# Kernel optimization log

Hardware: AMD Instinct MI355X
Metric: run time of the kernel (lower is better)

Reference implementation:

```python
import jax, jax.numpy as jnp
import numpy as np

PAD = 0
V, D = 50000, 300
MUS = np.array([-0.9, -0.7, -0.5, -0.3, -0.1, 0.1, 0.3, 0.5, 0.7, 0.9, 1.0], dtype=np.float32)
SIGMAS = np.array([0.1] * 10 + [0.001], dtype=np.float32)


def setup_inputs() -> dict:
    key = jax.random.key(0)
    k1, k2, k3, k4, k5, k6, k7 = jax.random.split(key, 7)
    B, Q, T = 256, 16, 1024
    return {
        "posdoc": jax.random.randint(k1, (B, T), 0, V),
        "negdoc": jax.random.randint(k2, (B, T), 0, V),
        "query": jax.random.randint(k3, (B, Q), 0, V),
        "query_idf": jax.random.normal(k4, (B, Q), dtype=jnp.float32),
        "emb": jax.random.normal(k5, (V, D), dtype=jnp.float32) * 0.1,
        "mus": jnp.asarray(MUS),
        "sigmas": jnp.asarray(SIGMAS),
        "W": jax.random.normal(k6, (11, 1), dtype=jnp.float32) * 0.3,
        "b": jax.random.normal(k7, (1,), dtype=jnp.float32) * 0.01,
    }


def _get_score(doc_tok, query_tok, emb, mus, sigmas, W, b):
    q = emb[query_tok]                                    # [B,Q,D]
    d = emb[doc_tok]                                      # [B,T,D]
    qn = q / (jnp.linalg.norm(q, axis=-1, keepdims=True) + 1e-9)
    dn = d / (jnp.linalg.norm(d, axis=-1, keepdims=True) + 1e-9)
    sim = jnp.einsum('bqd,btd->bqt', qn, dn)              # cosine simmat [B,Q,T]
    pair_mask = (query_tok != PAD)[:, :, None] & (doc_tok != PAD)[:, None, :]
    sim = sim * pair_mask                                 # zero out pad pairs
    # RBF kernel bank: [B,K,Q,T]
    diff = sim[:, None, :, :] - mus[None, :, None, None]
    k = jnp.exp(-0.5 * diff * diff / (sigmas[None, :, None, None] ** 2))
    doc_k = jnp.sum(k, axis=3)                            # [B,K,Q]
    qmask = jnp.sum(sim, axis=2) != 0.0                   # [B,Q]
    log_k = jnp.where(qmask[:, None, :], jnp.log(doc_k + 1e-6), 0.0)
    query_k = jnp.sum(log_k, axis=2)                      # [B,K]
    return (query_k @ W + b)[:, 0]                        # [B]


def reference(posdoc, negdoc, query, query_idf, emb, mus, sigmas, W, b):
    pos = _get_score(posdoc, query, emb, mus, sigmas, W, b)
    neg = _get_score(negdoc, query, emb, mus, sigmas, W, b)
    return jnp.stack([pos, neg], axis=1)                  # [B,2]
```

## Files before the change

kernel.cpp:

```cpp
#include <hip/hip_runtime.h>
#include <math.h>

#define BQ 16
#define TT 1024
#define DD 300
#define KK 11
#define ND4 75
#define KPAD 320
#define NCH 4

typedef unsigned short u16;
typedef unsigned char u8;
typedef long long i64;
typedef float f32x4 __attribute__((ext_vector_type(4)));

__device__ __forceinline__ unsigned f2e4m3(float f) {
    unsigned u = __float_as_uint(f);
    unsigned s = (u >> 24) & 0x80u;
    float a = fabsf(f);
    unsigned code;
    if (a < 0.015625f) {
        code = (unsigned)(int)rintf(a * 512.0f);
    } else {
        unsigned au = u & 0x7fffffffu;
        au += 0x7ffffu + ((au >> 20) & 1u);
        int e32 = (int)(au >> 23) - 127;
        code = ((unsigned)(e32 + 7) << 3) | ((au >> 20) & 7u);
    }
    return s | code;
}

__global__ __launch_bounds__(256) void knrm_norm_table(
    const float* __restrict__ emb, u8* __restrict__ table, int V)
{
    const int tid = threadIdx.x;
    const int sub = tid & 15;
    const int row = blockIdx.x * 16 + (tid >> 4);
    if (row >= V) return;

    const float4* __restrict__ src = (const float4*)(emb + (size_t)row * DD);
    float4 v[5];
    float ssq = 0.f;
    #pragma unroll
    for (int it = 0; it < 5; ++it) {
        int j = sub + 16 * it;
        if (j < ND4) {
            v[it] = src[j];
            ssq += v[it].x * v[it].x + v[it].y * v[it].y
                 + v[it].z * v[it].z + v[it].w * v[it].w;
        } else {
            v[it] = make_float4(0.f, 0.f, 0.f, 0.f);
        }
    }
    #pragma unroll
    for (int off = 8; off; off >>= 1) ssq += __shfl_xor(ssq, off, 16);
    const float inv = (row == 0) ? 0.f : 1.f / (sqrtf(ssq) + 1e-9f);

    unsigned* __restrict__ dst = (unsigned*)(table + (size_t)row * KPAD);
    #pragma unroll
    for (int it = 0; it < 5; ++it) {
        int j = sub + 16 * it;
        unsigned w = f2e4m3(v[it].x * inv)
                   | (f2e4m3(v[it].y * inv) << 8)
                   | (f2e4m3(v[it].z * inv) << 16)
                   | (f2e4m3(v[it].w * inv) << 24);
        dst[j] = w;
    }
}

__global__ __launch_bounds__(256, 4) void knrm_mfma(
    const int* __restrict__ posdoc, const int* __restrict__ negdoc,
    const int* __restrict__ query,
    const u8* __restrict__ table,
    const float* __restrict__ mus, const float* __restrict__ sigmas,
    float* __restrict__ part)
{
    __shared__ float red[4][BQ][12];

    const int bid   = blockIdx.x;
    const int pair  = bid >> 2;
    const int chunk = bid & 3;
    const int bb    = pair >> 1;
    const int* __restrict__ doc = (pair & 1) ? negdoc : posdoc;
    const int tid  = threadIdx.x;
    const int lane = tid & 63;
    const int wave = tid >> 6;
    const int quad = lane >> 4;
    const int m    = lane & 15;

    const int qtok = query[bb * BQ + m];
    const i64* __restrict__ ap = (const i64*)(table + (size_t)qtok * KPAD + quad * 8);
    i64 afr[10];
    #pragma unroll
    for (int ks = 0; ks < 10; ++ks) afr[ks] = ap[ks * 4];

    const int tbase = bb * TT + chunk * 256 + wave * 64 + m;
    int toks[4];
    #pragma unroll
    for (int t = 0; t < 4; ++t) toks[t] = doc[tbase + t * 16];

    float muk[10], ck[10];
    #pragma unroll
    for (int k = 0; k < 10; ++k) {
        muk[k] = mus[k];
        float sg = sigmas[k];
        ck[k] = -0.72134752f / (sg * sg);
    }

    float vacc[12][4];
    #pragma unroll
    for (int v = 0; v < 12; ++v)
        #pragma unroll
        for (int r = 0; r < 4; ++r) vacc[v][r] = 0.f;

    #pragma unroll
    for (int tp = 0; tp < 2; ++tp) {
        const i64* __restrict__ bp0 =
            (const i64*)(table + (size_t)toks[2 * tp]     * KPAD + quad * 8);
        const i64* __restrict__ bp1 =
            (const i64*)(table + (size_t)toks[2 * tp + 1] * KPAD + quad * 8);
        i64 b0[10], b1[10];
        #pragma unroll
        for (int ks = 0; ks < 10; ++ks) { b0[ks] = bp0[ks * 4]; b1[ks] = bp1[ks * 4]; }

        f32x4 acc0 = {0.f, 0.f, 0.f, 0.f};
        f32x4 acc1 = {0.f, 0.f, 0.f, 0.f};
        #pragma unroll
        for (int ks = 0; ks < 10; ++ks) {
            acc0 = __builtin_amdgcn_mfma_f32_16x16x32_fp8_fp8(afr[ks], b0[ks], acc0, 0, 0, 0);
            acc1 = __builtin_amdgcn_mfma_f32_16x16x32_fp8_fp8(afr[ks], b1[ks], acc1, 0, 0, 0);
        }

        #pragma unroll
        for (int r = 0; r < 4; ++r) {
            float s0 = acc0[r], s1 = acc1[r];
            vacc[11][r] += s0 + s1;
            vacc[10][r] += (s0 > 0.9f ? 1.f : 0.f)
                         + (s1 > 0.9f ? 1.f : 0.f);
            #pragma unroll
            for (int k = 0; k < 10; ++k) {
                float d0 = s0 - muk[k], d1 = s1 - muk[k];
                vacc[k][r] += __builtin_amdgcn_exp2f(ck[k] * d0 * d0)
                            + __builtin_amdgcn_exp2f(ck[k] * d1 * d1);
            }
        }
    }

    #pragma unroll
    for (int r = 0; r < 4; ++r) {
        #pragma unroll
        for (int off = 8; off; off >>= 1)
            #pragma unroll
            for (int v = 0; v < 12; ++v)
                vacc[v][r] += __shfl_down(vacc[v][r], off, 16);
        if (m == 0) {
            int q = quad * 4 + r;
            #pragma unroll
            for (int v = 0; v < 12; ++v) red[wave][q][v] = vacc[v][r];
        }
    }
    __syncthreads();

    if (tid < 192) {
        int v = tid >> 4, q = tid & 15;
        float sum = red[0][q][v] + red[1][q][v] + red[2][q][v] + red[3][q][v];
        part[((size_t)bid * 12 + v) * BQ + q] = sum;
    }
}

__global__ __launch_bounds__(256) void knrm_partial(
    const int* __restrict__ posdoc, const int* __restrict__ negdoc,
    const int* __restrict__ query,
    const float* __restrict__ emb,
    const float* __restrict__ mus, const float* __restrict__ sigmas,
    float* __restrict__ ws)
{
    __shared__ __align__(16) float qs[BQ * DD];
    __shared__ float qscale[BQ];

    const int bid   = blockIdx.x;
    const int pair  = bid >> 2;
    const int chunk = bid & 3;
    const int bb    = pair >> 1;
    const int sel   = pair & 1;
    const int* __restrict__ doc = sel ? negdoc : posdoc;
    const int tid  = threadIdx.x;
    const int lane = tid & 63;
    const int wave = tid >> 6;

    float4* qs4 = (float4*)qs;
    for (int idx = tid; idx < BQ * ND4; idx += 256) {
        int q   = idx / ND4;
        int c   = idx - q * ND4;
        int tok = query[bb * BQ + q];
        qs4[idx] = ((const float4*)(emb + (size_t)tok * DD))[c];
    }
    __syncthreads();
    {
        int q = tid >> 4, sub = tid & 15;
        float ssq = 0.f;
        for (int i = sub; i < DD; i += 16) { float v = qs[q * DD + i]; ssq += v * v; }
        #pragma unroll
        for (int off = 8; off; off >>= 1) ssq += __shfl_down(ssq, off, 16);
        if (sub == 0) {
            int tok = query[bb * BQ + q];
            qscale[q] = (tok == 0) ? 0.f : 1.f / (sqrtf(ssq) + 1e-9f);
        }
    }
    __syncthreads();
    for (int idx = tid; idx < BQ * ND4; idx += 256) {
        int q = idx / ND4;
        float sc = qscale[q];
        float4 v = qs4[idx];
        v.x *= sc; v.y *= sc; v.z *= sc; v.w *= sc;
        qs4[idx] = v;
    }
    __syncthreads();

    const int tok = doc[bb * TT + chunk * 256 + tid];
    const float4* __restrict__ rowp = (const float4*)(emb + (size_t)tok * DD);
    float acc[BQ];
    #pragma unroll
    for (int q = 0; q < BQ; ++q) acc[q] = 0.f;
    float dss = 0.f;
    #pragma unroll 5
    for (int d4 = 0; d4 < ND4; ++d4) {
        float4 dv = rowp[d4];
        dss += dv.x * dv.x + dv.y * dv.y + dv.z * dv.z + dv.w * dv.w;
        #pragma unroll
        for (int q = 0; q < BQ; ++q) {
            float4 qv = qs4[q * ND4 + d4];
            acc[q] += dv.x * qv.x + dv.y * qv.y + dv.z * qv.z + dv.w * qv.w;
        }
    }
    const float invd = (tok == 0) ? 0.f : 1.f / (sqrtf(dss) + 1e-9f);

    float muk[KK], ck[KK];
    #pragma unroll
    for (int k = 0; k < KK; ++k) {
        muk[k] = mus[k];
        float sg = sigmas[k];
        ck[k] = -0.72134752f / (sg * sg);
    }
    __syncthreads();
    float* red = qs;
    const int grp = wave * 4 + (lane >> 4);
    const bool wr = (lane & 15) == 0;
    for (int q = 0; q < BQ; ++q) {
        float s = acc[q] * invd;
        float vals[12];
        vals[11] = s;
        #pragma unroll
        for (int k = 0; k < KK; ++k) {
            float d = s - muk[k];
            vals[k] = __builtin_amdgcn_exp2f(ck[k] * d * d);
        }
        #pragma unroll
        for (int off = 8; off; off >>= 1)
            #pragma unroll
            for (int v = 0; v < 12; ++v)
                vals[v] += __shfl_down(vals[v], off, 16);
        if (wr) {
            #pragma unroll
            for (int v = 0; v < 12; ++v) red[(grp * BQ + q) * 12 + v] = vals[v];
        }
    }
    __syncthreads();
    if (tid < 192) {
        int v = tid >> 4, q = tid & 15;
        float sum = 0.f;
        #pragma unroll
        for (int g = 0; g < 16; ++g) sum += red[(g * BQ + q) * 12 + v];
        ws[((size_t)(pair * 4 + chunk) * 12 + v) * BQ + q] = sum;
    }
}

__global__ __launch_bounds__(192) void knrm_final(
    const float* __restrict__ part,
    const float* __restrict__ Wv, const float* __restrict__ bv,
    float* __restrict__ out, int nchunk)
{
    __shared__ float dock[12 * BQ];
    __shared__ float lsum[KK];
    const int pair = blockIdx.x;
    const int tid  = threadIdx.x;
    {
        int v = tid >> 4, q = tid & 15;
        float sum = 0.f;
        for (int c = 0; c < nchunk; ++c)
            sum += part[((size_t)(pair * nchunk + c) * 12 + v) * BQ + q];
        dock[v * BQ + q] = sum;
    }
    __syncthreads();
    if (tid < 176) {
        int k = tid >> 4, q = tid & 15;
        float qm = dock[11 * BQ + q];
        float lv = (qm != 0.0f) ? logf(dock[k * BQ + q] + 1e-6f) : 0.f;
        #pragma unroll
        for (int off = 8; off; off >>= 1) lv += __shfl_down(lv, off, 16);
        if (q == 0) lsum[k] = lv;
    }
    __syncthreads();
    if (tid == 0) {
        float sc = bv[0];
        #pragma unroll
        for (int k = 0; k < KK; ++k) sc += lsum[k] * Wv[k];
        out[pair] = sc;
    }
}

extern "C" void kernel_launch(void* const* d_in, const int* in_sizes, int n_in,
                              void* d_out, int out_size, void* d_ws, size_t ws_size,
                              hipStream_t stream) {
    const int*   posdoc = (const int*)  d_in[0];
    const int*   negdoc = (const int*)  d_in[1];
    const int*   query  = (const int*)  d_in[2];
    const float* emb    = (const float*)d_in[4];
    const float* mus    = (const float*)d_in[5];
    const float* sigmas = (const float*)d_in[6];
    const float* Wv     = (const float*)d_in[7];
    const float* bv     = (const float*)d_in[8];
    float* out = (float*)d_out;

    const int V = in_sizes[4] / DD;
    const size_t table_bytes = (size_t)V * KPAD;
    const size_t part_bytes  = (size_t)512 * NCH * 12 * BQ * sizeof(float);

    if (ws_size >= table_bytes + part_bytes) {
        u8*    table = (u8*)d_ws;
        float* part  = (float*)((char*)d_ws + table_bytes);
        knrm_norm_table<<<dim3((V + 15) / 16), dim3(256), 0, stream>>>(emb, table, V);
        knrm_mfma<<<dim3(512 * NCH), dim3(256), 0, stream>>>(
            posdoc, negdoc, query, table, mus, sigmas, part);
        knrm_final<<<dim3(512), dim3(192), 0, stream>>>(part, Wv, bv, out, NCH);
    } else {
        float* part = (float*)d_ws;
        knrm_partial<<<dim3(512 * 4), dim3(256), 0, stream>>>(
            posdoc, negdoc, query, emb, mus, sigmas, part);
        knrm_final<<<dim3(512), dim3(192), 0, stream>>>(part, Wv, bv, out, 4);
    }
}
```

Before: 155.3 us.

## Permute FP8 table layout for 16-byte loads and double-buffer doc fragments

The normalized FP8 embedding table is written in a permuted order so each lane's MFMA K-fragments sit contiguously. Each lane can then fetch them with five 16-byte loads instead of ten 8-byte strided loads. The doc-token loop now handles one token group at a time and software-prefetches the next group's fragments into a second register buffer while the current MFMAs and exp work run. This trades the two independent MFMA chains of the old loop for one chain per token, which could expose more MFMA latency, but it aims to cut load instruction count and improve load/compute overlap.

Measured after the change: 181.1 us. 16.6% more time.

```diff
diff --git a/kernel.cpp b/kernel.cpp
--- a/kernel.cpp
+++ b/kernel.cpp
@@ -13,6 +13,7 @@
 typedef unsigned char u8;
 typedef long long i64;
 typedef float f32x4 __attribute__((ext_vector_type(4)));
+typedef long long i64x2 __attribute__((ext_vector_type(2)));
 
 __device__ __forceinline__ unsigned f2e4m3(float f) {
     unsigned u = __float_as_uint(f);
@@ -64,7 +65,10 @@
                    | (f2e4m3(v[it].y * inv) << 8)
                    | (f2e4m3(v[it].z * inv) << 16)
                    | (f2e4m3(v[it].w * inv) << 24);
-        dst[j] = w;
+        int quad = (j >> 1) & 3;
+        int ks   = j >> 3;
+        int d    = quad * 20 + ks * 2 + (j & 1);
+        dst[d] = w;
     }
 }
 
@@ -88,16 +92,20 @@
     const int quad = lane >> 4;
     const int m    = lane & 15;
 
-    const int qtok = query[bb * BQ + m];
-    const i64* __restrict__ ap = (const i64*)(table + (size_t)qtok * KPAD + quad * 8);
-    i64 afr[10];
-    #pragma unroll
-    for (int ks = 0; ks < 10; ++ks) afr[ks] = ap[ks * 4];
-
     const int tbase = bb * TT + chunk * 256 + wave * 64 + m;
     int toks[4];
     #pragma unroll
     for (int t = 0; t < 4; ++t) toks[t] = doc[tbase + t * 16];
+    const i64x2* __restrict__ bp[4];
+    #pragma unroll
+    for (int t = 0; t < 4; ++t)
+        bp[t] = (const i64x2*)(table + (size_t)toks[t] * KPAD + quad * 80);
+
+    const int qtok = query[bb * BQ + m];
+    const i64x2* __restrict__ ap = (const i64x2*)(table + (size_t)qtok * KPAD + quad * 80);
+    i64x2 afr[5];
+    #pragma unroll
+    for (int g = 0; g < 5; ++g) afr[g] = ap[g];
 
     float muk[10], ck[10];
     #pragma unroll
@@ -113,35 +121,32 @@
         #pragma unroll
         for (int r = 0; r < 4; ++r) vacc[v][r] = 0.f;
 
-    #pragma unroll
-    for (int tp = 0; tp < 2; ++tp) {
-        const i64* __restrict__ bp0 =
-            (const i64*)(table + (size_t)toks[2 * tp]     * KPAD + quad * 8);
-        const i64* __restrict__ bp1 =
-            (const i64*)(table + (size_t)toks[2 * tp + 1] * KPAD + quad * 8);
-        i64 b0[10], b1[10];
-        #pragma unroll
-        for (int ks = 0; ks < 10; ++ks) { b0[ks] = bp0[ks * 4]; b1[ks] = bp1[ks * 4]; }
-
-        f32x4 acc0 = {0.f, 0.f, 0.f, 0.f};
-        f32x4 acc1 = {0.f, 0.f, 0.f, 0.f};
-        #pragma unroll
-        for (int ks = 0; ks < 10; ++ks) {
-            acc0 = __builtin_amdgcn_mfma_f32_16x16x32_fp8_fp8(afr[ks], b0[ks], acc0, 0, 0, 0);
-            acc1 = __builtin_amdgcn_mfma_f32_16x16x32_fp8_fp8(afr[ks], b1[ks], acc1, 0, 0, 0);
-        }
-
+    i64x2 bbuf[2][5];
+    #pragma unroll
+    for (int g = 0; g < 5; ++g) bbuf[0][g] = bp[0][g];
+
+    #pragma unroll
+    for (int t = 0; t < 4; ++t) {
+        const int cur = t & 1;
+        if (t < 3) {
+            #pragma unroll
+            for (int g = 0; g < 5; ++g) bbuf[cur ^ 1][g] = bp[t + 1][g];
+        }
+        f32x4 acc = {0.f, 0.f, 0.f, 0.f};
+        #pragma unroll
+        for (int g = 0; g < 5; ++g) {
+            acc = __builtin_amdgcn_mfma_f32_16x16x32_fp8_fp8(afr[g].x, bbuf[cur][g].x, acc, 0, 0, 0);
+            acc = __builtin_amdgcn_mfma_f32_16x16x32_fp8_fp8(afr[g].y, bbuf[cur][g].y, acc, 0, 0, 0);
+        }
         #pragma unroll
         for (int r = 0; r < 4; ++r) {
-            float s0 = acc0[r], s1 = acc1[r];
-            vacc[11][r] += s0 + s1;
-            vacc[10][r] += (s0 > 0.9f ? 1.f : 0.f)
-                         + (s1 > 0.9f ? 1.f : 0.f);
+            float s = acc[r];
+            vacc[11][r] += s;
+            vacc[10][r] += (s > 0.9f ? 1.f : 0.f);
             #pragma unroll
             for (int k = 0; k < 10; ++k) {
-                float d0 = s0 - muk[k], d1 = s1 - muk[k];
-                vacc[k][r] += __builtin_amdgcn_exp2f(ck[k] * d0 * d0)
-                            + __builtin_amdgcn_exp2f(ck[k] * d1 * d1);
+                float d = s - muk[k];
+                vacc[k][r] += __builtin_amdgcn_exp2f(ck[k] * d * d);
             }
         }
     }
```

## Software-pipeline doc tile loads with inline asm and one-wave-per-row norm table

Applied to the files above, without the earlier changes.

The MFMA kernel now issues doc-embedding loads with explicit inline-asm global loads into two rotating register buffers and uses manual vmcnt waits, so the next tile's loads are in flight while the current tile's MFMAs and RBF exponentials run. Occupancy hint drops from 4 to 3 blocks per SIMD to make room for the extra buffered registers. The norm-table kernel is reorganised to one wave per embedding row with a full-wave shuffle reduction, and now explicitly zeroes the padding bytes. The risks are fewer resident waves, and fragile manual vmcnt accounting that depends on the compiler not inserting other loads in between.

Result: faster. 151.1 us (-2.7%).

```diff
diff --git a/kernel.cpp b/kernel.cpp
--- a/kernel.cpp
+++ b/kernel.cpp
@@ -30,45 +30,54 @@
     return s | code;
 }
 
+template<int OFF>
+__device__ __forceinline__ void gload8(i64& dst, const u8* p) {
+    asm volatile("global_load_dwordx2 %0, %1, off offset:%2"
+                 : "=v"(dst) : "v"(p), "i"(OFF));
+}
+
+#define ISSUE_TILE(B, P)                                                    \
+    gload8<0>((B)[0], P);   gload8<32>((B)[1], P);  gload8<64>((B)[2], P);  \
+    gload8<96>((B)[3], P);  gload8<128>((B)[4], P); gload8<160>((B)[5], P); \
+    gload8<192>((B)[6], P); gload8<224>((B)[7], P); gload8<256>((B)[8], P); \
+    gload8<288>((B)[9], P);
+
+#define TILE_WAIT(NSTR, B)                                                  \
+    asm volatile("s_waitcnt vmcnt(" NSTR ")"                                \
+        : "+v"((B)[0]), "+v"((B)[1]), "+v"((B)[2]), "+v"((B)[3]),           \
+          "+v"((B)[4]), "+v"((B)[5]), "+v"((B)[6]), "+v"((B)[7]),           \
+          "+v"((B)[8]), "+v"((B)[9]))
+
 __global__ __launch_bounds__(256) void knrm_norm_table(
     const float* __restrict__ emb, u8* __restrict__ table, int V)
 {
-    const int tid = threadIdx.x;
-    const int sub = tid & 15;
-    const int row = blockIdx.x * 16 + (tid >> 4);
-    if (row >= V) return;
-
-    const float4* __restrict__ src = (const float4*)(emb + (size_t)row * DD);
-    float4 v[5];
-    float ssq = 0.f;
-    #pragma unroll
-    for (int it = 0; it < 5; ++it) {
-        int j = sub + 16 * it;
-        if (j < ND4) {
-            v[it] = src[j];
-            ssq += v[it].x * v[it].x + v[it].y * v[it].y
-                 + v[it].z * v[it].z + v[it].w * v[it].w;
-        } else {
-            v[it] = make_float4(0.f, 0.f, 0.f, 0.f);
-        }
-    }
-    #pragma unroll
-    for (int off = 8; off; off >>= 1) ssq += __shfl_xor(ssq, off, 16);
-    const float inv = (row == 0) ? 0.f : 1.f / (sqrtf(ssq) + 1e-9f);
-
-    unsigned* __restrict__ dst = (unsigned*)(table + (size_t)row * KPAD);
-    #pragma unroll
-    for (int it = 0; it < 5; ++it) {
-        int j = sub + 16 * it;
-        unsigned w = f2e4m3(v[it].x * inv)
-                   | (f2e4m3(v[it].y * inv) << 8)
-                   | (f2e4m3(v[it].z * inv) << 16)
-                   | (f2e4m3(v[it].w * inv) << 24);
-        dst[j] = w;
-    }
-}
-
-__global__ __launch_bounds__(256, 4) void knrm_mfma(
+    const int w    = (blockIdx.x * 256 + threadIdx.x) >> 6;
+    const int lane = threadIdx.x & 63;
+    if (w >= V) return;
+
+    const float4* __restrict__ src = (const float4*)(emb + (size_t)w * DD);
+    float4 v = make_float4(0.f, 0.f, 0.f, 0.f);
+    float4 v2 = v;
+    if (lane < ND4) v = src[lane];
+    if (lane < ND4 - 64) v2 = src[64 + lane];
+    float ssq = v.x * v.x + v.y * v.y + v.z * v.z + v.w * v.w
+              + v2.x * v2.x + v2.y * v2.y + v2.z * v2.z + v2.w * v2.w;
+    #pragma unroll
+    for (int off = 32; off; off >>= 1) ssq += __shfl_xor(ssq, off);
+    const float inv = (w == 0) ? 0.f : 1.f / (sqrtf(ssq) + 1e-9f);
+
+    unsigned* __restrict__ dst = (unsigned*)(table + (size_t)w * KPAD);
+    unsigned p = f2e4m3(v.x * inv) | (f2e4m3(v.y * inv) << 8)
+               | (f2e4m3(v.z * inv) << 16) | (f2e4m3(v.w * inv) << 24);
+    dst[lane] = (lane < ND4) ? p : 0u;
+    if (lane < 16) {
+        unsigned p2 = f2e4m3(v2.x * inv) | (f2e4m3(v2.y * inv) << 8)
+                    | (f2e4m3(v2.z * inv) << 16) | (f2e4m3(v2.w * inv) << 24);
+        dst[64 + lane] = (lane < ND4 - 64) ? p2 : 0u;
+    }
+}
+
+__global__ __launch_bounds__(256, 3) void knrm_mfma(
     const int* __restrict__ posdoc, const int* __restrict__ negdoc,
     const int* __restrict__ query,
     const u8* __restrict__ table,
@@ -88,16 +97,20 @@
     const int quad = lane >> 4;
     const int m    = lane & 15;
 
+    const int tbase = bb * TT + chunk * 256 + wave * 64 + m;
+    int toks[4];
+    #pragma unroll
+    for (int t = 0; t < 4; ++t) toks[t] = doc[tbase + t * 16];
+    const u8* bp0 = table + (size_t)toks[0] * KPAD + quad * 8;
+    const u8* bp1 = table + (size_t)toks[1] * KPAD + quad * 8;
+    const u8* bp2 = table + (size_t)toks[2] * KPAD + quad * 8;
+    const u8* bp3 = table + (size_t)toks[3] * KPAD + quad * 8;
+
     const int qtok = query[bb * BQ + m];
     const i64* __restrict__ ap = (const i64*)(table + (size_t)qtok * KPAD + quad * 8);
     i64 afr[10];
     #pragma unroll
     for (int ks = 0; ks < 10; ++ks) afr[ks] = ap[ks * 4];
-
-    const int tbase = bb * TT + chunk * 256 + wave * 64 + m;
-    int toks[4];
-    #pragma unroll
-    for (int t = 0; t < 4; ++t) toks[t] = doc[tbase + t * 16];
 
     float muk[10], ck[10];
     #pragma unroll
@@ -113,38 +126,44 @@
         #pragma unroll
         for (int r = 0; r < 4; ++r) vacc[v][r] = 0.f;
 
-    #pragma unroll
-    for (int tp = 0; tp < 2; ++tp) {
-        const i64* __restrict__ bp0 =
-            (const i64*)(table + (size_t)toks[2 * tp]     * KPAD + quad * 8);
-        const i64* __restrict__ bp1 =
-            (const i64*)(table + (size_t)toks[2 * tp + 1] * KPAD + quad * 8);
-        i64 b0[10], b1[10];
-        #pragma unroll
-        for (int ks = 0; ks < 10; ++ks) { b0[ks] = bp0[ks * 4]; b1[ks] = bp1[ks * 4]; }
-
-        f32x4 acc0 = {0.f, 0.f, 0.f, 0.f};
-        f32x4 acc1 = {0.f, 0.f, 0.f, 0.f};
-        #pragma unroll
-        for (int ks = 0; ks < 10; ++ks) {
-            acc0 = __builtin_amdgcn_mfma_f32_16x16x32_fp8_fp8(afr[ks], b0[ks], acc0, 0, 0, 0);
-            acc1 = __builtin_amdgcn_mfma_f32_16x16x32_fp8_fp8(afr[ks], b1[ks], acc1, 0, 0, 0);
-        }
-
-        #pragma unroll
-        for (int r = 0; r < 4; ++r) {
-            float s0 = acc0[r], s1 = acc1[r];
-            vacc[11][r] += s0 + s1;
-            vacc[10][r] += (s0 > 0.9f ? 1.f : 0.f)
-                         + (s1 > 0.9f ? 1.f : 0.f);
-            #pragma unroll
-            for (int k = 0; k < 10; ++k) {
-                float d0 = s0 - muk[k], d1 = s1 - muk[k];
-                vacc[k][r] += __builtin_amdgcn_exp2f(ck[k] * d0 * d0)
-                            + __builtin_amdgcn_exp2f(ck[k] * d1 * d1);
-            }
-        }
-    }
+    asm volatile("s_waitcnt vmcnt(0)"
+        : "+v"(afr[0]), "+v"(afr[1]), "+v"(afr[2]), "+v"(afr[3]), "+v"(afr[4]),
+          "+v"(afr[5]), "+v"(afr[6]), "+v"(afr[7]), "+v"(afr[8]), "+v"(afr[9]));
+
+    i64 ba[10], bbuf[10];
+    ISSUE_TILE(ba, bp0);
+    ISSUE_TILE(bbuf, bp1);
+
+    #define COMPUTE_TILE(B)                                                        \
+    {                                                                              \
+        f32x4 acc = {0.f, 0.f, 0.f, 0.f};                                          \
+        _Pragma("unroll")                                                          \
+        for (int g = 0; g < 10; ++g)                                               \
+            acc = __builtin_amdgcn_mfma_f32_16x16x32_fp8_fp8(afr[g], (B)[g], acc, 0, 0, 0); \
+        _Pragma("unroll")                                                          \
+        for (int r = 0; r < 4; ++r) {                                              \
+            float s = acc[r];                                                      \
+            vacc[11][r] += s;                                                      \
+            vacc[10][r] += (s > 0.9f ? 1.f : 0.f);                                 \
+            _Pragma("unroll")                                                      \
+            for (int k = 0; k < 10; ++k) {                                         \
+                float d = s - muk[k];                                              \
+                vacc[k][r] += __builtin_amdgcn_exp2f(ck[k] * d * d);               \
+            }                                                                      \
+        }                                                                          \
+    }
+
+    TILE_WAIT("10", ba);
+    COMPUTE_TILE(ba);
+    ISSUE_TILE(ba, bp2);
+    TILE_WAIT("10", bbuf);
+    COMPUTE_TILE(bbuf);
+    ISSUE_TILE(bbuf, bp3);
+    TILE_WAIT("10", ba);
+    COMPUTE_TILE(ba);
+    TILE_WAIT("0", bbuf);
+    COMPUTE_TILE(bbuf);
+    #undef COMPUTE_TILE
 
     #pragma unroll
     for (int r = 0; r < 4; ++r) {
@@ -329,7 +348,7 @@
     if (ws_size >= table_bytes + part_bytes) {
         u8*    table = (u8*)d_ws;
         float* part  = (float*)((char*)d_ws + table_bytes);
-        knrm_norm_table<<<dim3((V + 15) / 16), dim3(256), 0, stream>>>(emb, table, V);
+        knrm_norm_table<<<dim3((V + 3) / 4), dim3(256), 0, stream>>>(emb, table, V);
         knrm_mfma<<<dim3(512 * NCH), dim3(256), 0, stream>>>(
             posdoc, negdoc, query, table, mus, sigmas, part);
         knrm_final<<<dim3(512), dim3(192), 0, stream>>>(part, Wv, bv, out, NCH);
```
